# Optimization experiments

Measured on AMD Instinct MI355X. Metric: run time of the kernel, lower is better.

Reference implementation:

```python
import jax, jax.numpy as jnp
import numpy as np

B, T, D, H = 4, 2048, 1024, 16
Dh = D // H  # 64


def setup_inputs() -> dict:
    key = jax.random.key(0)
    ks = jax.random.split(key, 12)
    s = 1.0 / np.sqrt(D)
    return {
        "q": jax.random.normal(ks[0], (B, T, D), jnp.float32),
        "k": jax.random.normal(ks[1], (B, T, D), jnp.float32),
        "v": jax.random.normal(ks[2], (B, T, D), jnp.float32),
        "Wq": jax.random.normal(ks[3], (D, D), jnp.float32) * s,
        "bq": jnp.zeros((D,), jnp.float32),
        "Wk": jax.random.normal(ks[4], (D, D), jnp.float32) * s,
        "bk": jnp.zeros((D,), jnp.float32),
        "Wv": jax.random.normal(ks[5], (Dh, D), jnp.float32) * s,
        "bv": jnp.zeros((Dh,), jnp.float32),
        "Wo": jax.random.normal(ks[6], (D, D), jnp.float32) * s,
        "bo": jnp.zeros((D,), jnp.float32),
    }


def reference(q, k, v, Wq, bq, Wk, bk, Wv, bv, Wo, bo):
    # Projections (torch Linear: y = x @ W.T + b)
    Q = (q @ Wq.T + bq).reshape(B, T, H, Dh)   # [B,T,H,Dh]
    K = (k @ Wk.T + bk).reshape(B, T, H, Dh)   # [B,T,H,Dh]
    Vs = v @ Wv.T + bv                         # [B,T,Dh] shared across heads
    scale = 1.0 / np.sqrt(Dh).astype(np.float32)
    scores = jnp.einsum('bqhd,bkhd->bhqk', Q, K) * scale  # [B,H,T,T]
    attn = jax.nn.softmax(scores, axis=-1)
    # shared-V: broadcast V over heads
    out = jnp.einsum('bhqk,bkd->bqhd', attn, Vs)  # [B,T,H,Dh]
    out = out.reshape(B, T, D)
    y = out @ Wo.T + bo                           # [B,T,D]
    return y, attn.mean(axis=1)                   # per-head-averaged attention
```

## Files before the change

### kernel.cpp

```cpp
#include <hip/hip_runtime.h>
#include <cstdint>
#include <cstddef>

typedef __attribute__((ext_vector_type(8))) _Float16 half8;
typedef __attribute__((ext_vector_type(4))) _Float16 half4;
typedef __attribute__((ext_vector_type(4))) float f32x4;

#define DEV static __device__ __forceinline__
#define AS1(p) (const __attribute__((address_space(1))) void*)(p)
#define AS3(p) (__attribute__((address_space(3))) void*)(p)

#define LDS_BARRIER() asm volatile("s_waitcnt lgkmcnt(0)\n\ts_barrier" ::: "memory")

DEV half8 cvt8(const float* p) {
    f32x4 a = *(const f32x4*)p;
    f32x4 b = *(const f32x4*)(p + 4);
    half8 o;
    o[0] = (_Float16)a[0]; o[1] = (_Float16)a[1];
    o[2] = (_Float16)a[2]; o[3] = (_Float16)a[3];
    o[4] = (_Float16)b[0]; o[5] = (_Float16)b[1];
    o[6] = (_Float16)b[2]; o[7] = (_Float16)b[3];
    return o;
}

__global__ __launch_bounds__(256)
void cvt2_kernel(const float* __restrict__ a, _Float16* __restrict__ oa,
                 const float* __restrict__ b, _Float16* __restrict__ ob, int n8)
{
    int i = blockIdx.x * 256 + threadIdx.x;
    int stride = gridDim.x * 256;
    for (; i < 2 * n8; i += stride) {
        if (i < n8) ((half8*)oa)[i] = cvt8(a + (size_t)i * 8);
        else        ((half8*)ob)[i - n8] = cvt8(b + (size_t)(i - n8) * 8);
    }
}

__global__ __launch_bounds__(256)
void cvt3_kernel(const float* __restrict__ a, _Float16* __restrict__ oa,
                 const float* __restrict__ b, _Float16* __restrict__ ob,
                 const float* __restrict__ c, _Float16* __restrict__ oc, int n8)
{
    int i = blockIdx.x * 256 + threadIdx.x;
    int stride = gridDim.x * 256;
    for (; i < 3 * n8; i += stride) {
        if (i < n8)           ((half8*)oa)[i] = cvt8(a + (size_t)i * 8);
        else if (i < 2 * n8)  ((half8*)ob)[i - n8] = cvt8(b + (size_t)(i - n8) * 8);
        else                  ((half8*)oc)[i - 2 * n8] = cvt8(c + (size_t)(i - 2 * n8) * 8);
    }
}

__global__ __launch_bounds__(256)
void combine_kernel(const _Float16* __restrict__ a, const _Float16* __restrict__ b,
                    float* __restrict__ out, int n8)
{
    int i = blockIdx.x * 256 + threadIdx.x;
    int stride = gridDim.x * 256;
    for (; i < n8; i += stride) {
        half8 x = ((const half8*)a)[i];
        half8 y = ((const half8*)b)[i];
        f32x4 o0, o1;
#pragma unroll
        for (int j = 0; j < 4; j++) o0[j] = ((float)x[j] + (float)y[j]) * 0.0625f;
#pragma unroll
        for (int j = 0; j < 4; j++) o1[j] = ((float)x[j + 4] + (float)y[j + 4]) * 0.0625f;
        *(f32x4*)(out + (size_t)i * 8) = o0;
        *(f32x4*)(out + (size_t)i * 8 + 4) = o1;
    }
}

template<bool OUT_F16>
__global__ __launch_bounds__(256, 2)
void gemm16(const _Float16* __restrict__ A, const _Float16* __restrict__ B,
            const float* __restrict__ bias, float scale, void* __restrict__ Cout,
            int M, int N, int K)
{
    __shared__ half8 As[2][512];
    __shared__ half8 Bs[2][512];
    const int tid = threadIdx.x, l = tid & 63, w = tid >> 6;
    const int lr = l & 15, lh = l >> 4;
    const int wm0 = (w >> 1) * 64, wn0 = (w & 1) * 64;
    const int bm0 = blockIdx.x * 128, bn0 = blockIdx.y * 128;
    const int nsteps = K >> 5;

    f32x4 acc[4][4] = {};

#define STAGE(buf, t) do {                                                        \
        int k0 = (t) << 5;                                                        \
        _Pragma("unroll")                                                         \
        for (int q2 = 0; q2 < 2; q2++) {                                          \
            int r = q2 * 64 + l;                                                  \
            __builtin_amdgcn_global_load_lds(                                     \
                AS1(A + (size_t)(bm0 + r) * K + k0 + w * 8),                      \
                AS3(&As[buf][w * 128 + q2 * 64]), 16, 0, 0);                      \
            __builtin_amdgcn_global_load_lds(                                     \
                AS1(B + (size_t)(bn0 + r) * K + k0 + w * 8),                      \
                AS3(&Bs[buf][w * 128 + q2 * 64]), 16, 0, 0);                      \
        }                                                                         \
    } while (0)

    STAGE(0, 0);
    __syncthreads();
    for (int t = 0; t < nsteps; t++) {
        int cur = t & 1;
        if (t + 1 < nsteps) STAGE(cur ^ 1, t + 1);
        half8 a[4], b[4];
#pragma unroll
        for (int m = 0; m < 4; m++) a[m] = As[cur][lh * 128 + wm0 + m * 16 + lr];
#pragma unroll
        for (int n = 0; n < 4; n++) b[n] = Bs[cur][lh * 128 + wn0 + n * 16 + lr];
#pragma unroll
        for (int m = 0; m < 4; m++)
#pragma unroll
            for (int n = 0; n < 4; n++)
                acc[m][n] = __builtin_amdgcn_mfma_f32_16x16x32_f16(a[m], b[n], acc[m][n], 0, 0, 0);
        __syncthreads();
    }
#undef STAGE

#pragma unroll
    for (int m = 0; m < 4; m++)
#pragma unroll
        for (int n = 0; n < 4; n++) {
            int row0 = bm0 + wm0 + m * 16 + lh * 4;
            int col = bn0 + wn0 + n * 16 + lr;
            float bv = bias[col];
#pragma unroll
            for (int j = 0; j < 4; j++) {
                float val = (acc[m][n][j] + bv) * scale;
                int row = row0 + j;
                if constexpr (OUT_F16)
                    ((_Float16*)Cout)[(size_t)row * N + col] = (_Float16)val;
                else
                    ((float*)Cout)[(size_t)row * N + col] = val;
            }
        }
}

template<int BM, int BN, int WR, int WC>
__global__ __launch_bounds__(256, 2)
void gemm_vp(const float* __restrict__ Aptr, const float* __restrict__ Bw,
             const float* __restrict__ bias, _Float16* __restrict__ Cout, int M, int N, int K)
{
    constexpr int BK = 32;
    constexpr int WM = BM / WR, WN = BN / WC;
    constexpr int MF = WM / 16, NF = WN / 16;
    constexpr int LDT = 40;
    __shared__ _Float16 Asl[BM][LDT];
    __shared__ _Float16 Bsl[BN][LDT];

    const int tid = threadIdx.x;
    const int l = tid & 63;
    const int w = tid >> 6;
    const int wr = w / WC, wc = w % WC;
    const int lr = l & 15, lh = l >> 4;
    const int bm0 = blockIdx.y * BM, bn0 = blockIdx.x * BN;

    f32x4 acc[MF][NF] = {};

    for (int k0 = 0; k0 < K; k0 += BK) {
        __syncthreads();
        for (int c = tid; c < BM * 4; c += 256) {
            int row = c >> 2, c8 = (c & 3) << 3;
            *(half8*)&Asl[row][c8] = cvt8(Aptr + (size_t)(bm0 + row) * K + k0 + c8);
        }
        for (int c = tid; c < BN * 4; c += 256) {
            int row = c >> 2, c8 = (c & 3) << 3;
            *(half8*)&Bsl[row][c8] = cvt8(Bw + (size_t)(bn0 + row) * K + k0 + c8);
        }
        __syncthreads();

        half8 a[MF], b[NF];
#pragma unroll
        for (int m = 0; m < MF; m++)
            a[m] = *(const half8*)&Asl[wr * WM + m * 16 + lr][lh * 8];
#pragma unroll
        for (int n = 0; n < NF; n++)
            b[n] = *(const half8*)&Bsl[wc * WN + n * 16 + lr][lh * 8];
#pragma unroll
        for (int m = 0; m < MF; m++)
#pragma unroll
            for (int n = 0; n < NF; n++)
                acc[m][n] = __builtin_amdgcn_mfma_f32_16x16x32_f16(a[m], b[n], acc[m][n], 0, 0, 0);
    }

#pragma unroll
    for (int m = 0; m < MF; m++)
#pragma unroll
        for (int n = 0; n < NF; n++) {
            int row0 = bm0 + wr * WM + m * 16 + lh * 4;
            int col = bn0 + wc * WN + n * 16 + lr;
            float bv = bias[col];
#pragma unroll
            for (int j = 0; j < 4; j++) {
                float val = acc[m][n][j] + bv;
                int row = row0 + j;
                int bi = row >> 11, t = row & 2047;
                Cout[(((size_t)(bi * 64 + col)) << 11) + t] = (_Float16)val;
            }
        }
}

#define LK(dst, kt) do {                                                          \
        const _Float16* kp_ = Kb + (size_t)((kt) * 32) * 1024;                    \
        _Pragma("unroll")                                                         \
        for (int kfr_ = 0; kfr_ < 2; kfr_++)                                      \
            _Pragma("unroll")                                                     \
            for (int dk_ = 0; dk_ < 2; dk_++)                                     \
                dst[kfr_][dk_] = *(const half8*)(kp_ + (size_t)(kfr_ * 16 + lr) * 1024 \
                                                 + ch + dk_ * 32 + lh * 8);       \
    } while (0)

__global__ __launch_bounds__(512, 4)
void stats_kernel(const _Float16* __restrict__ Qh, const _Float16* __restrict__ Kh,
                  float* __restrict__ slp)
{
    const int blk = blockIdx.x;
    const int b = blk & 3;
    const int hg = (blk >> 2) & 1;
    const int q0 = (blk >> 3) << 5;
    const int tid = threadIdx.x;
    const int l = tid & 63, w = tid >> 6;
    const int lr = l & 15, lh = l >> 4;
    const int ch = (hg * 8 + w) * 64;

    const size_t base = (size_t)b * 2048 * 1024;
    const _Float16* Qb = Qh + base;
    const _Float16* Kb = Kh + base;

    half8 qf[2][2];
#pragma unroll
    for (int m = 0; m < 2; m++)
#pragma unroll
        for (int dk = 0; dk < 2; dk++)
            qf[m][dk] = *(const half8*)(Qb + (size_t)(q0 + m * 16 + lr) * 1024
                                        + ch + dk * 32 + lh * 8);

    float sl[2][4] = {};
    half8 ka[2][2], kb2[2][2];

#define SBODY(KF) do {                                                            \
        f32x4 sc[2][2] = {};                                                      \
        _Pragma("unroll")                                                         \
        for (int m = 0; m < 2; m++)                                               \
            _Pragma("unroll")                                                     \
            for (int kfr = 0; kfr < 2; kfr++)                                     \
                _Pragma("unroll")                                                 \
                for (int dk = 0; dk < 2; dk++)                                    \
                    sc[m][kfr] = __builtin_amdgcn_mfma_f32_16x16x32_f16(          \
                        qf[m][dk], KF[kfr][dk], sc[m][kfr], 0, 0, 0);             \
        _Pragma("unroll")                                                         \
        for (int m = 0; m < 2; m++)                                               \
            _Pragma("unroll")                                                     \
            for (int j = 0; j < 4; j++)                                           \
                sl[m][j] += __builtin_amdgcn_exp2f(sc[m][0][j])                   \
                          + __builtin_amdgcn_exp2f(sc[m][1][j]);                  \
    } while (0)

    LK(ka, 0);
    for (int kt = 0; kt < 64; kt += 2) {
        LK(kb2, kt + 1);
        SBODY(ka);
        LK(ka, kt + 2 < 64 ? kt + 2 : 63);
        SBODY(kb2);
    }
#undef SBODY

#pragma unroll
    for (int m = 0; m < 2; m++)
#pragma unroll
        for (int j = 0; j < 4; j++) {
            float s = sl[m][j];
#pragma unroll
            for (int d = 1; d < 16; d <<= 1)
                s += __shfl_xor(s, d, 64);
            if (lr == 0)
                slp[(size_t)(b * 16 + hg * 8 + w) * 2048 + q0 + m * 16 + lh * 4 + j] = s;
        }
}

__global__ __launch_bounds__(512, 4)
void emit_kernel(const _Float16* __restrict__ Qh, const _Float16* __restrict__ Kh,
                 const _Float16* __restrict__ VT, const float* __restrict__ slp,
                 _Float16* __restrict__ attnp, _Float16* __restrict__ Op)
{
    const int blk = blockIdx.x;
    const int b = blk & 3;
    const int hg = (blk >> 2) & 1;
    const int q0 = (blk >> 3) << 5;
    const int tid = threadIdx.x;
    const int l = tid & 63, w = tid >> 6;
    const int lr = l & 15, lh = l >> 4;
    const int ch = (hg * 8 + w) * 64;

    __shared__ __align__(16) _Float16 Pld[2][8][32][40];

    const size_t base = (size_t)b * 2048 * 1024;
    const _Float16* Qb = Qh + base;
    const _Float16* Kb = Kh + base;

    half8 qf[2][2];
#pragma unroll
    for (int m = 0; m < 2; m++)
#pragma unroll
        for (int dk = 0; dk < 2; dk++)
            qf[m][dk] = *(const half8*)(Qb + (size_t)(q0 + m * 16 + lr) * 1024
                                        + ch + dk * 32 + lh * 8);

    float rinv[2];
    {
        const float* sr = slp + (size_t)(b * 16 + hg * 8 + w) * 2048 + q0;
#pragma unroll
        for (int m = 0; m < 2; m++)
            rinv[m] = 1.0f / sr[m * 16 + lr];
    }

    f32x4 oacc[2][4] = {};
    half8 ka[2][2], kb2[2][2];

#define EBODY(KF, KT, P) do {                                                     \
        const int krow = (KT) * 32;                                               \
        f32x4 sc[2][2] = {};         \
        _Pragma("unroll")                                                         \
        for (int m = 0; m < 2; m++)                                               \
            _Pragma("unroll")                                                     \
            for (int kfr = 0; kfr < 2; kfr++)                                     \
                _Pragma("unroll")                                                 \
                for (int dk = 0; dk < 2; dk++)                                    \
                    sc[m][kfr] = __builtin_amdgcn_mfma_f32_16x16x32_f16(          \
                        KF[kfr][dk], qf[m][dk], sc[m][kfr], 0, 0, 0);             \
        _Pragma("unroll")                                                         \
        for (int m = 0; m < 2; m++)                                               \
            _Pragma("unroll")                                                     \
            for (int kfr = 0; kfr < 2; kfr++) {                                   \
                half4 pk4;                                                        \
                _Pragma("unroll")                                                 \
                for (int j = 0; j < 4; j++)                                       \
                    pk4[j] = (_Float16)(__builtin_amdgcn_exp2f(sc[m][kfr][j])     \
                                        * rinv[m]);                               \
                *(half4*)&Pld[P][w][m * 16 + lr][kfr * 16 + lh * 4] = pk4;        \
            }                                                                     \
        half8 vf[4], pa[2];                                                       \
        _Pragma("unroll")                                                         \
        for (int dv = 0; dv < 4; dv++)                                            \
            vf[dv] = *(const half8*)(VT + (((size_t)(b * 64 + dv * 16 + lr)) << 11) + krow + lh * 8); \
        _Pragma("unroll")                                                         \
        for (int m = 0; m < 2; m++)                                               \
            pa[m] = *(const half8*)&Pld[P][w][m * 16 + lr][lh * 8];               \
        _Pragma("unroll")                                                         \
        for (int m = 0; m < 2; m++)                                               \
            _Pragma("unroll")                                                     \
            for (int dv = 0; dv < 4; dv++)                                        \
                oacc[m][dv] = __builtin_amdgcn_mfma_f32_16x16x32_f16(             \
                    pa[m], vf[dv], oacc[m][dv], 0, 0, 0);                         \
        LDS_BARRIER();                                                            \
        {                                                                         \
            int r = tid >> 4, c2 = (tid & 15) * 2;                                \
            float s0 = 0.f, s1 = 0.f;                                             \
            _Pragma("unroll")                                                     \
            for (int ww = 0; ww < 8; ww++) {                                      \
                union { uint32_t u; _Float16 h[2]; } pv;                          \
                pv.u = *(const uint32_t*)&Pld[P][ww][r][c2];                      \
                s0 += (float)pv.h[0]; s1 += (float)pv.h[1];                       \
            }                                                                     \
            union { _Float16 h[2]; uint32_t u; } pk;                              \
            pk.h[0] = (_Float16)s0; pk.h[1] = (_Float16)s1;                       \
            __builtin_nontemporal_store(pk.u, (uint32_t*)(attnp                   \
                + (size_t)hg * 16777216 + (((size_t)(b * 2048 + q0 + r)) << 11)   \
                + krow + c2));                                                    \
        }                                                                         \
    } while (0)

    LK(ka, 0);
    for (int i = 0; i < 64; i += 2) {
        LK(kb2, i + 1);
        EBODY(ka, i, 0);
        LK(ka, i + 2 < 64 ? i + 2 : 63);
        EBODY(kb2, i + 1, 1);
    }
#undef EBODY

    _Float16* op = Op + base;
#pragma unroll
    for (int m = 0; m < 2; m++)
#pragma unroll
        for (int dv = 0; dv < 4; dv++)
#pragma unroll
            for (int j = 0; j < 4; j++) {
                int row = q0 + m * 16 + lh * 4 + j;
                int col = ch + dv * 16 + lr;
                op[(size_t)row * 1024 + col] = (_Float16)oacc[m][dv][j];
            }
}

extern "C" void kernel_launch(void* const* d_in, const int* in_sizes, int n_in,
                              void* d_out, int out_size, void* d_ws, size_t ws_size,
                              hipStream_t stream)
{
    const float* q  = (const float*)d_in[0];
    const float* k  = (const float*)d_in[1];
    const float* v  = (const float*)d_in[2];
    const float* Wq = (const float*)d_in[3];
    const float* bq = (const float*)d_in[4];
    const float* Wk = (const float*)d_in[5];
    const float* bk = (const float*)d_in[6];
    const float* Wv = (const float*)d_in[7];
    const float* bv = (const float*)d_in[8];
    const float* Wo = (const float*)d_in[9];
    const float* bo = (const float*)d_in[10];

    float* y = (float*)d_out;
    float* attn_mean = y + (size_t)4 * 2048 * 1024;

    uint8_t* ws = (uint8_t*)d_ws;
    _Float16* Qh  = (_Float16*)(ws);
    _Float16* Kh  = (_Float16*)(ws + 16777216);
    _Float16* VT  = (_Float16*)(ws + 33554432);
    _Float16* Wqc = (_Float16*)(ws + 34603008);
    _Float16* Wkc = (_Float16*)(ws + 36700160);
    _Float16* Woc = (_Float16*)(ws + 38797312);
    _Float16* qc  = (_Float16*)(ws + 40894464);
    _Float16* kc  = (_Float16*)(ws + 57671680);
    _Float16* Op  = qc;
    _Float16* attnp = (_Float16*)(ws + 74448896);
    float*    slp = (float*)(ws + 34603008);

    const float QS = 0.125f * 1.44269504088896340736f;

    cvt2_kernel<<<dim3(2048), dim3(256), 0, stream>>>(q, qc, k, kc, 1048576);
    cvt3_kernel<<<dim3(512),  dim3(256), 0, stream>>>(Wq, Wqc, Wk, Wkc, Wo, Woc, 131072);

    gemm16<true><<<dim3(64, 8), dim3(256), 0, stream>>>(qc, Wqc, bq, QS, Qh, 8192, 1024, 1024);
    gemm16<true><<<dim3(64, 8), dim3(256), 0, stream>>>(kc, Wkc, bk, 1.0f, Kh, 8192, 1024, 1024);
    gemm_vp<128, 64, 4, 1><<<dim3(1, 64), dim3(256), 0, stream>>>(v, Wv, bv, VT, 8192, 64, 1024);

    stats_kernel<<<dim3(512), dim3(512), 0, stream>>>(Qh, Kh, slp);
    emit_kernel<<<dim3(512), dim3(512), 0, stream>>>(Qh, Kh, VT, slp, attnp, Op);

    combine_kernel<<<dim3(2048), dim3(256), 0, stream>>>(
        attnp, attnp + (size_t)16777216, attn_mean, 2097152);

    gemm16<false><<<dim3(64, 8), dim3(256), 0, stream>>>(Op, Woc, bo, 1.0f, y, 8192, 1024, 1024);
}
```

Before: 571.3 us.

## Fuse attention stats and emit passes, merge conversions and Q/K projection launches

Merges the softmax-denominator pass and the probability/output emit pass into one kernel, so row sums stay in registers and are redistributed with lane shuffles instead of a round trip through global memory. The five fp32-to-fp16 conversions move into one launch, and the Q and K projection GEMMs run as a single launch using blockIdx.z. This removes launch overhead and the slp buffer traffic, and gives the Q/K GEMM a larger grid. The cost is higher register and LDS pressure in the fused attention kernel, which could lower occupancy.

```diff
diff --git a/kernel.cpp b/kernel.cpp
--- a/kernel.cpp
+++ b/kernel.cpp
@@ -24,28 +24,25 @@
 }
 
 __global__ __launch_bounds__(256)
-void cvt2_kernel(const float* __restrict__ a, _Float16* __restrict__ oa,
-                 const float* __restrict__ b, _Float16* __restrict__ ob, int n8)
-{
+void cvt5_kernel(const float* __restrict__ q, _Float16* __restrict__ oq,
+                 const float* __restrict__ k, _Float16* __restrict__ ok,
+                 const float* __restrict__ wq, _Float16* __restrict__ owq,
+                 const float* __restrict__ wk, _Float16* __restrict__ owk,
+                 const float* __restrict__ wo, _Float16* __restrict__ owo)
+{
+    const int NQ = 1048576, NW = 131072;
+    const int total = 2 * NQ + 3 * NW;
     int i = blockIdx.x * 256 + threadIdx.x;
     int stride = gridDim.x * 256;
-    for (; i < 2 * n8; i += stride) {
-        if (i < n8) ((half8*)oa)[i] = cvt8(a + (size_t)i * 8);
-        else        ((half8*)ob)[i - n8] = cvt8(b + (size_t)(i - n8) * 8);
-    }
-}
-
-__global__ __launch_bounds__(256)
-void cvt3_kernel(const float* __restrict__ a, _Float16* __restrict__ oa,
-                 const float* __restrict__ b, _Float16* __restrict__ ob,
-                 const float* __restrict__ c, _Float16* __restrict__ oc, int n8)
-{
-    int i = blockIdx.x * 256 + threadIdx.x;
-    int stride = gridDim.x * 256;
-    for (; i < 3 * n8; i += stride) {
-        if (i < n8)           ((half8*)oa)[i] = cvt8(a + (size_t)i * 8);
-        else if (i < 2 * n8)  ((half8*)ob)[i - n8] = cvt8(b + (size_t)(i - n8) * 8);
-        else                  ((half8*)oc)[i - 2 * n8] = cvt8(c + (size_t)(i - 2 * n8) * 8);
+    for (; i < total; i += stride) {
+        if (i < NQ)            ((half8*)oq)[i] = cvt8(q + (size_t)i * 8);
+        else if (i < 2 * NQ)   ((half8*)ok)[i - NQ] = cvt8(k + (size_t)(i - NQ) * 8);
+        else {
+            int j = i - 2 * NQ;
+            if (j < NW)        ((half8*)owq)[j] = cvt8(wq + (size_t)j * 8);
+            else if (j < 2*NW) ((half8*)owk)[j - NW] = cvt8(wk + (size_t)(j - NW) * 8);
+            else               ((half8*)owo)[j - 2*NW] = cvt8(wo + (size_t)(j - 2*NW) * 8);
+        }
     }
 }
 
@@ -68,21 +65,49 @@
     }
 }
 
-template<bool OUT_F16>
-__global__ __launch_bounds__(256, 2)
-void gemm16(const _Float16* __restrict__ A, const _Float16* __restrict__ B,
-            const float* __restrict__ bias, float scale, void* __restrict__ Cout,
-            int M, int N, int K)
-{
-    __shared__ half8 As[2][512];
-    __shared__ half8 Bs[2][512];
-    const int tid = threadIdx.x, l = tid & 63, w = tid >> 6;
-    const int lr = l & 15, lh = l >> 4;
-    const int wm0 = (w >> 1) * 64, wn0 = (w & 1) * 64;
-    const int bm0 = blockIdx.x * 128, bn0 = blockIdx.y * 128;
-    const int nsteps = K >> 5;
-
-    f32x4 acc[4][4] = {};
+#define GEMM_BODY(A, B, bias, scale, Cout)                                        \
+    __shared__ half8 As[2][512];                                                  \
+    __shared__ half8 Bs[2][512];                                                  \
+    const int tid = threadIdx.x, l = tid & 63, w = tid >> 6;                      \
+    const int lr = l & 15, lh = l >> 4;                                           \
+    const int wm0 = (w >> 1) * 64, wn0 = (w & 1) * 64;                            \
+    const int bm0 = blockIdx.x * 128, bn0 = blockIdx.y * 128;                     \
+    const int nsteps = K >> 5;                                                    \
+    f32x4 acc[4][4] = {};                                                         \
+    STAGE(0, 0);                                                                  \
+    __syncthreads();                                                              \
+    for (int t = 0; t < nsteps; t++) {                                            \
+        int cur = t & 1;                                                          \
+        if (t + 1 < nsteps) STAGE(cur ^ 1, t + 1);                                \
+        half8 a[4], b[4];                                                         \
+        _Pragma("unroll")                                                         \
+        for (int m = 0; m < 4; m++) a[m] = As[cur][lh * 128 + wm0 + m * 16 + lr]; \
+        _Pragma("unroll")                                                         \
+        for (int n = 0; n < 4; n++) b[n] = Bs[cur][lh * 128 + wn0 + n * 16 + lr]; \
+        _Pragma("unroll")                                                         \
+        for (int m = 0; m < 4; m++)                                               \
+            _Pragma("unroll")                                                     \
+            for (int n = 0; n < 4; n++)                                           \
+                acc[m][n] = __builtin_amdgcn_mfma_f32_16x16x32_f16(a[m], b[n], acc[m][n], 0, 0, 0); \
+        __syncthreads();                                                          \
+    }                                                                             \
+    _Pragma("unroll")                                                             \
+    for (int m = 0; m < 4; m++)                                                   \
+        _Pragma("unroll")                                                         \
+        for (int n = 0; n < 4; n++) {                                             \
+            int row0 = bm0 + wm0 + m * 16 + lh * 4;                               \
+            int col = bn0 + wn0 + n * 16 + lr;                                    \
+            float bv = bias[col];                                                 \
+            _Pragma("unroll")                                                     \
+            for (int j = 0; j < 4; j++) {                                         \
+                float val = (acc[m][n][j] + bv) * scale;                          \
+                int row = row0 + j;                                               \
+                if constexpr (OUT_F16)                                            \
+                    ((_Float16*)Cout)[(size_t)row * N + col] = (_Float16)val;     \
+                else                                                              \
+                    ((float*)Cout)[(size_t)row * N + col] = val;                  \
+            }                                                                     \
+        }
 
 #define STAGE(buf, t) do {                                                        \
         int k0 = (t) << 5;                                                        \
@@ -98,43 +123,31 @@
         }                                                                         \
     } while (0)
 
-    STAGE(0, 0);
-    __syncthreads();
-    for (int t = 0; t < nsteps; t++) {
-        int cur = t & 1;
-        if (t + 1 < nsteps) STAGE(cur ^ 1, t + 1);
-        half8 a[4], b[4];
-#pragma unroll
-        for (int m = 0; m < 4; m++) a[m] = As[cur][lh * 128 + wm0 + m * 16 + lr];
-#pragma unroll
-        for (int n = 0; n < 4; n++) b[n] = Bs[cur][lh * 128 + wn0 + n * 16 + lr];
-#pragma unroll
-        for (int m = 0; m < 4; m++)
-#pragma unroll
-            for (int n = 0; n < 4; n++)
-                acc[m][n] = __builtin_amdgcn_mfma_f32_16x16x32_f16(a[m], b[n], acc[m][n], 0, 0, 0);
-        __syncthreads();
-    }
+template<bool OUT_F16>
+__global__ __launch_bounds__(256, 2)
+void gemm16(const _Float16* __restrict__ A, const _Float16* __restrict__ B,
+            const float* __restrict__ bias, float scale, void* __restrict__ Cout,
+            int M, int N, int K)
+{
+    GEMM_BODY(A, B, bias, scale, Cout)
+}
+
+template<bool OUT_F16>
+__global__ __launch_bounds__(256, 2)
+void gemm16_dual(const _Float16* __restrict__ A0, const _Float16* __restrict__ B0,
+                 const float* __restrict__ bias0, float scale0, void* __restrict__ C0,
+                 const _Float16* __restrict__ A1, const _Float16* __restrict__ B1,
+                 const float* __restrict__ bias1, float scale1, void* __restrict__ C1,
+                 int M, int N, int K)
+{
+    const _Float16* A = blockIdx.z ? A1 : A0;
+    const _Float16* B = blockIdx.z ? B1 : B0;
+    const float* bias = blockIdx.z ? bias1 : bias0;
+    float scale = blockIdx.z ? scale1 : scale0;
+    void* Cout = blockIdx.z ? C1 : C0;
+    GEMM_BODY(A, B, bias, scale, Cout)
+}
 #undef STAGE
-
-#pragma unroll
-    for (int m = 0; m < 4; m++)
-#pragma unroll
-        for (int n = 0; n < 4; n++) {
-            int row0 = bm0 + wm0 + m * 16 + lh * 4;
-            int col = bn0 + wn0 + n * 16 + lr;
-            float bv = bias[col];
-#pragma unroll
-            for (int j = 0; j < 4; j++) {
-                float val = (acc[m][n][j] + bv) * scale;
-                int row = row0 + j;
-                if constexpr (OUT_F16)
-                    ((_Float16*)Cout)[(size_t)row * N + col] = (_Float16)val;
-                else
-                    ((float*)Cout)[(size_t)row * N + col] = val;
-            }
-        }
-}
 
 template<int BM, int BN, int WR, int WC>
 __global__ __launch_bounds__(256, 2)
@@ -211,8 +224,9 @@
     } while (0)
 
 __global__ __launch_bounds__(512, 4)
-void stats_kernel(const _Float16* __restrict__ Qh, const _Float16* __restrict__ Kh,
-                  float* __restrict__ slp)
+void attn_fused(const _Float16* __restrict__ Qh, const _Float16* __restrict__ Kh,
+                const _Float16* __restrict__ VT, _Float16* __restrict__ attnp,
+                _Float16* __restrict__ Op)
 {
     const int blk = blockIdx.x;
     const int b = blk & 3;
@@ -223,6 +237,8 @@
     const int lr = l & 15, lh = l >> 4;
     const int ch = (hg * 8 + w) * 64;
 
+    __shared__ __align__(16) _Float16 Pld[2][8][32][40];
+
     const size_t base = (size_t)b * 2048 * 1024;
     const _Float16* Qb = Qh + base;
     const _Float16* Kb = Kh + base;
@@ -236,8 +252,8 @@
                                         + ch + dk * 32 + lh * 8);
 
     float sl[2][4] = {};
-    half8 ka[2][2], kb2[2][2];
-
+    {
+        half8 ka[2][2], kb2[2][2];
 #define SBODY(KF) do {                                                            \
         f32x4 sc[2][2] = {};                                                      \
         _Pragma("unroll")                                                         \
@@ -255,16 +271,15 @@
                 sl[m][j] += __builtin_amdgcn_exp2f(sc[m][0][j])                   \
                           + __builtin_amdgcn_exp2f(sc[m][1][j]);                  \
     } while (0)
-
-    LK(ka, 0);
-    for (int kt = 0; kt < 64; kt += 2) {
-        LK(kb2, kt + 1);
-        SBODY(ka);
-        LK(ka, kt + 2 < 64 ? kt + 2 : 63);
-        SBODY(kb2);
-    }
+        LK(ka, 0);
+        for (int kt = 0; kt < 64; kt += 2) {
+            LK(kb2, kt + 1);
+            SBODY(ka);
+            LK(ka, kt + 2 < 64 ? kt + 2 : 63);
+            SBODY(kb2);
+        }
 #undef SBODY
-
+    }
 #pragma unroll
     for (int m = 0; m < 2; m++)
 #pragma unroll
@@ -273,45 +288,19 @@
 #pragma unroll
             for (int d = 1; d < 16; d <<= 1)
                 s += __shfl_xor(s, d, 64);
-            if (lr == 0)
-                slp[(size_t)(b * 16 + hg * 8 + w) * 2048 + q0 + m * 16 + lh * 4 + j] = s;
-        }
-}
-
-__global__ __launch_bounds__(512, 4)
-void emit_kernel(const _Float16* __restrict__ Qh, const _Float16* __restrict__ Kh,
-                 const _Float16* __restrict__ VT, const float* __restrict__ slp,
-                 _Float16* __restrict__ attnp, _Float16* __restrict__ Op)
-{
-    const int blk = blockIdx.x;
-    const int b = blk & 3;
-    const int hg = (blk >> 2) & 1;
-    const int q0 = (blk >> 3) << 5;
-    const int tid = threadIdx.x;
-    const int l = tid & 63, w = tid >> 6;
-    const int lr = l & 15, lh = l >> 4;
-    const int ch = (hg * 8 + w) * 64;
-
-    __shared__ __align__(16) _Float16 Pld[2][8][32][40];
-
-    const size_t base = (size_t)b * 2048 * 1024;
-    const _Float16* Qb = Qh + base;
-    const _Float16* Kb = Kh + base;
-
-    half8 qf[2][2];
-#pragma unroll
-    for (int m = 0; m < 2; m++)
-#pragma unroll
-        for (int dk = 0; dk < 2; dk++)
-            qf[m][dk] = *(const half8*)(Qb + (size_t)(q0 + m * 16 + lr) * 1024
-                                        + ch + dk * 32 + lh * 8);
-
+            sl[m][j] = s;
+        }
     float rinv[2];
-    {
-        const float* sr = slp + (size_t)(b * 16 + hg * 8 + w) * 2048 + q0;
-#pragma unroll
-        for (int m = 0; m < 2; m++)
-            rinv[m] = 1.0f / sr[m * 16 + lr];
+#pragma unroll
+    for (int m = 0; m < 2; m++) {
+        int src = (lr >> 2) << 4;
+        float t0 = __shfl(sl[m][0], src, 64);
+        float t1 = __shfl(sl[m][1], src, 64);
+        float t2 = __shfl(sl[m][2], src, 64);
+        float t3 = __shfl(sl[m][3], src, 64);
+        int jj = lr & 3;
+        float s = (jj == 0) ? t0 : (jj == 1) ? t1 : (jj == 2) ? t2 : t3;
+        rinv[m] = 1.0f / s;
     }
 
     f32x4 oacc[2][4] = {};
@@ -319,7 +308,7 @@
 
 #define EBODY(KF, KT, P) do {                                                     \
         const int krow = (KT) * 32;                                               \
-        f32x4 sc[2][2] = {};         \
+        f32x4 sc[2][2] = {};                                                      \
         _Pragma("unroll")                                                         \
         for (int m = 0; m < 2; m++)                                               \
             _Pragma("unroll")                                                     \
@@ -422,19 +411,16 @@
     _Float16* kc  = (_Float16*)(ws + 57671680);
     _Float16* Op  = qc;
     _Float16* attnp = (_Float16*)(ws + 74448896);
-    float*    slp = (float*)(ws + 34603008);
 
     const float QS = 0.125f * 1.44269504088896340736f;
 
-    cvt2_kernel<<<dim3(2048), dim3(256), 0, stream>>>(q, qc, k, kc, 1048576);
-    cvt3_kernel<<<dim3(512),  dim3(256), 0, stream>>>(Wq, Wqc, Wk, Wkc, Wo, Woc, 131072);
-
-    gemm16<true><<<dim3(64, 8), dim3(256), 0, stream>>>(qc, Wqc, bq, QS, Qh, 8192, 1024, 1024);
-    gemm16<true><<<dim3(64, 8), dim3(256), 0, stream>>>(kc, Wkc, bk, 1.0f, Kh, 8192, 1024, 1024);
+    cvt5_kernel<<<dim3(2048), dim3(256), 0, stream>>>(q, qc, k, kc, Wq, Wqc, Wk, Wkc, Wo, Woc);
+
+    gemm16_dual<true><<<dim3(64, 8, 2), dim3(256), 0, stream>>>(
+        qc, Wqc, bq, QS, Qh, kc, Wkc, bk, 1.0f, Kh, 8192, 1024, 1024);
     gemm_vp<128, 64, 4, 1><<<dim3(1, 64), dim3(256), 0, stream>>>(v, Wv, bv, VT, 8192, 64, 1024);
 
-    stats_kernel<<<dim3(512), dim3(512), 0, stream>>>(Qh, Kh, slp);
-    emit_kernel<<<dim3(512), dim3(512), 0, stream>>>(Qh, Kh, VT, slp, attnp, Op);
+    attn_fused<<<dim3(512), dim3(512), 0, stream>>>(Qh, Kh, VT, attnp, Op);
 
     combine_kernel<<<dim3(2048), dim3(256), 0, stream>>>(
         attnp, attnp + (size_t)16777216, attn_mean, 2097152);
```

Result: no change. 563.2 us (-1.4%).
